# Kernel tuning notes

Measured on AMD Instinct MI355X. Metric: run time of the kernel, lower is better.

## Reference

```python
import jax, jax.numpy as jnp
import numpy as np

B, L, D = 2, 1024, 768
DEPTH, DI, N, K, R, FF = 6, 1536, 16, 4, 48, 3072  # d_inner=2*D, d_state, d_conv, dt_rank=D//16, ff=4*D


def setup_inputs() -> dict:
    key = jax.random.key(0)
    ks = iter(jax.random.split(key, 24))
    def rn(shape, sc=0.02):
        return jax.random.normal(next(ks), shape, dtype=jnp.float32) * sc
    return dict(
        x=rn((B, L, D), 1.0),
        ln1_w=jnp.ones((DEPTH, D), jnp.float32), ln1_b=jnp.zeros((DEPTH, D), jnp.float32),
        ln2_w=jnp.ones((DEPTH, D), jnp.float32), ln2_b=jnp.zeros((DEPTH, D), jnp.float32),
        in_w=rn((DEPTH, 2, 2 * DI, D)),
        conv_w=rn((DEPTH, 2, DI, K), 0.1), conv_b=jnp.zeros((DEPTH, 2, DI), jnp.float32),
        xproj_w=rn((DEPTH, 2, R + 2 * N, DI)),
        dtproj_w=rn((DEPTH, 2, DI, R), 0.1),
        dtproj_b=rn((DEPTH, 2, DI), 0.1),
        A_log=jnp.broadcast_to(jnp.log(jnp.arange(1, N + 1, dtype=jnp.float32)), (DEPTH, 2, DI, N)) + jnp.zeros((DEPTH, 2, DI, N), jnp.float32),
        D_param=jnp.ones((DEPTH, 2, DI), jnp.float32),
        out_w=rn((DEPTH, 2, D, DI)),
        mlp_w1=rn((DEPTH, FF, D)), mlp_b1=jnp.zeros((DEPTH, FF), jnp.float32),
        mlp_w2=rn((DEPTH, D, FF)), mlp_b2=jnp.zeros((DEPTH, D), jnp.float32),
    )


def _ln(x, w, b, eps=1e-5):
    m = x.mean(-1, keepdims=True)
    v = jnp.var(x, axis=-1, keepdims=True)
    return (x - m) * jax.lax.rsqrt(v + eps) * w + b


def _silu(x):
    return x * jax.nn.sigmoid(x)


def _mamba(x, in_w, conv_w, conv_b, xproj_w, dtproj_w, dtproj_b, A_log, Dp, out_w):
    b = x.shape[0]
    xz = jnp.einsum('bld,ed->ble', x, in_w)                    # (B,L,2*DI)
    xp, z = jnp.split(xz, 2, axis=-1)
    xt = jnp.transpose(xp, (0, 2, 1))                           # (B,DI,L)
    xc = jax.lax.conv_general_dilated(xt, conv_w[:, None, :], (1,), [(K - 1, 0)],
                                      dimension_numbers=('NCH', 'OIH', 'NCH'),
                                      feature_group_count=DI)   # causal depthwise conv
    xc = _silu(xc + conv_b[None, :, None])
    xc = jnp.transpose(xc, (0, 2, 1))                           # (B,L,DI)
    xdbl = jnp.einsum('bld,ed->ble', xc, xproj_w)               # (B,L,R+2N)
    dt_lr = xdbl[..., :R]                                       # low-rank dt (B,L,R)
    Bs = xdbl[..., R:R + N]
    Cs = xdbl[..., R + N:]
    dt = jax.nn.softplus(jnp.einsum('blr,dr->bld', dt_lr, dtproj_w) + dtproj_b)  # (B,L,DI)
    A = -jnp.exp(A_log)                                          # (DI,N)

    def step(h, inp):
        dt_t, b_t, c_t, x_t = inp                                # (B,DI),(B,N),(B,N),(B,DI)
        dA = jnp.exp(dt_t[:, :, None] * A)
        h = dA * h + dt_t[:, :, None] * b_t[:, None, :] * x_t[:, :, None]
        return h, jnp.einsum('bdn,bn->bd', h, c_t)

    h0 = jnp.zeros((b, DI, N), x.dtype)
    _, ys = jax.lax.scan(step, h0, (dt.transpose(1, 0, 2), Bs.transpose(1, 0, 2),
                                    Cs.transpose(1, 0, 2), xc.transpose(1, 0, 2)))
    y = ys.transpose(1, 0, 2) + xc * Dp                          # (B,L,DI)
    y = y * _silu(z)
    return jnp.einsum('bld,ed->ble', y, out_w), dt, dt_lr


def _encoder(x, ln1_w, ln1_b, ln2_w, ln2_b, in_w, conv_w, conv_b, xproj_w,
             dtproj_w, dtproj_b, A_log, D_param, out_w, mlp_w1, mlp_b1, mlp_w2, mlp_b2):
    residual = None
    xs, dts_all, dtlr_all = [], [], []
    for i in range(DEPTH):
        residual = x if residual is None else x + residual
        h = _ln(residual, ln1_w[i], ln1_b[i])
        def mp(d):
            return (in_w[i, d], conv_w[i, d], conv_b[i, d], xproj_w[i, d],
                    dtproj_w[i, d], dtproj_b[i, d], A_log[i, d], D_param[i, d], out_w[i, d])
        xf, dt_f, dtlr_f = _mamba(h, *mp(0))
        xr, dt_b, dtlr_b = _mamba(jnp.flip(h, 1), *mp(1))
        m = (xf + jnp.flip(xr, 1)) * 0.5                          # BiMamba average
        dts_all.append(jnp.stack([dt_f, dt_b], 0))                # dt_backward left reversed, as in source
        dtlr_all.append(jnp.stack([dtlr_f, dtlr_b], 0))
        residual = m + residual
        h2 = _ln(residual, ln2_w[i], ln2_b[i])
        hid = jax.nn.gelu(jnp.einsum('bld,fd->blf', h2, mlp_w1[i]) + mlp_b1[i], approximate=False)
        x = jnp.einsum('blf,df->bld', hid, mlp_w2[i]) + mlp_b2[i]
        xs.append(x)
    return x, jnp.stack(xs, 0), jnp.stack(dts_all, 0), jnp.stack(dtlr_all, 0)


def reference(x, ln1_w, ln1_b, ln2_w, ln2_b, in_w, conv_w, conv_b, xproj_w,
              dtproj_w, dtproj_b, A_log, D_param, out_w, mlp_w1, mlp_b1, mlp_w2, mlp_b2):
    return _encoder(x, ln1_w, ln1_b, ln2_w, ln2_b, in_w, conv_w, conv_b, xproj_w,
                    dtproj_w, dtproj_b, A_log, D_param, out_w, mlp_w1, mlp_b1, mlp_w2, mlp_b2)
```

## Files before the change

kernel.cpp:

```cpp
#include <hip/hip_runtime.h>
#include <cmath>

#define B_ 2
#define L_ 1024
#define D_ 768
#define DEPTH_ 6
#define DI_ 1536
#define NS_ 16
#define KC_ 4
#define R_ 48
#define FF_ 3072
#define BL_ (B_*L_)
#define XD_ 128
#define CH2_ 32
#define S_ 32

#define OUT_XS   ((size_t)BL_*D_)
#define OUT_DTS  (OUT_XS + (size_t)DEPTH_*BL_*D_)
#define OUT_DTLR (OUT_DTS + (size_t)DEPTH_*2*BL_*DI_)

typedef unsigned short u16;
typedef unsigned int u32;
typedef __bf16 bf16x8 __attribute__((ext_vector_type(8)));
typedef float f32x4 __attribute__((ext_vector_type(4)));

__device__ __forceinline__ float siluf(float x){ return x / (1.f + __expf(-x)); }
__device__ __forceinline__ float softplusf(float x){ return fmaxf(x,0.f) + log1pf(__expf(-fabsf(x))); }
__device__ __forceinline__ float geluf(float x){ return 0.5f*x*(1.f+erff(x*0.7071067811865475f)); }
__device__ __forceinline__ u32 f2bf(float f){
    u32 u = __float_as_uint(f);
    return (u + 0x7FFFu + ((u>>16)&1u)) >> 16;
}
__device__ __forceinline__ float bf2f(u16 v){ return __uint_as_float(((u32)v)<<16); }

__device__ __forceinline__ void cvt4(const float* __restrict__ in, u16* __restrict__ out, int i)
{
    float4 v = ((const float4*)in)[i];
    uint2 o;
    o.x = f2bf(v.x) | (f2bf(v.y) << 16);
    o.y = f2bf(v.z) | (f2bf(v.w) << 16);
    ((uint2*)out)[i] = o;
}

__global__ __launch_bounds__(256) void cvt_weights(
    const float* __restrict__ in_w, const float* __restrict__ out_w,
    const float* __restrict__ m1, const float* __restrict__ m2,
    const float* __restrict__ xp, const float* __restrict__ wdt,
    u16* __restrict__ w_in, u16* __restrict__ w_out, u16* __restrict__ w_m1,
    u16* __restrict__ w_m2, u16* __restrict__ w_xp, u16* __restrict__ w_dt)
{
    int seg = blockIdx.y;
    int i = blockIdx.x*256 + threadIdx.x;
    if (seg == 0) { if (i < 2*(2*DI_)*D_/4) cvt4(in_w, w_in, i); }
    else if (seg == 1) { if (i < 2*D_*DI_/4) cvt4(out_w, w_out, i); }
    else if (seg == 2) { if (i < FF_*D_/4) cvt4(m1, w_m1, i); }
    else if (seg == 3) { if (i < D_*FF_/4) cvt4(m2, w_m2, i); }
    else if (seg == 4) {
        if (i < 2*XD_*DI_/4) {
            int base = i*4;
            int k = base % DI_;
            int rr = (base/DI_) % XD_;
            int z = base/(DI_*XD_);
            uint2 o = {0u,0u};
            if (rr < 80) {
                float4 v = *(const float4*)&xp[((size_t)z*80 + rr)*DI_ + k];
                o.x = f2bf(v.x) | (f2bf(v.y) << 16);
                o.y = f2bf(v.z) | (f2bf(v.w) << 16);
            }
            ((uint2*)w_xp)[i] = o;
        }
    } else {
        if (i < 2*DI_*64/4) {
            int base = i*4;
            int c = base % 64;
            int r = (base/64) % DI_;
            int z = base/(64*DI_);
            uint2 o = {0u,0u};
            if (c < 48) {
                float4 v = *(const float4*)&wdt[((size_t)z*DI_ + r)*48 + c];
                o.x = f2bf(v.x) | (f2bf(v.y) << 16);
                o.y = f2bf(v.z) | (f2bf(v.w) << 16);
            }
            ((uint2*)w_dt)[i] = o;
        }
    }
}

template<int EPI, int OUTBF>
__global__ __launch_bounds__(256) void gemm_bf16(
    const u16* __restrict__ A, const u16* __restrict__ Bw,
    float* __restrict__ C, u16* __restrict__ Cbf, const float* __restrict__ bias,
    float* __restrict__ out2, int layer,
    int M, int N, int K, int KS, long aS, long bS, long cS, long biasS)
{
    const int zAll = blockIdx.z;
    const int sk = zAll % KS, zb = zAll / KS;
    A  += (size_t)zb * aS;
    Bw += (size_t)zb * bS;
    __shared__ u16 As[128*64];
    __shared__ u16 Bs[128*64];
    const int tid = threadIdx.x;
    const int w = tid >> 6, l = tid & 63;
    const int wr = w >> 1, wc = w & 1;
    const int row0 = blockIdx.x * 128, col0 = blockIdx.y * 128;
    const int Ksl = K / KS;
    const int kbeg = sk * Ksl;
    const int srow = l >> 3;
    const int scol = (l & 7) * 8;
    f32x4 acc[4][4] = {};
    for (int k0 = kbeg; k0 < kbeg + Ksl; k0 += 64) {
        #pragma unroll
        for (int c = 0; c < 4; ++c) {
            int chunk = w*4 + c;
            const u16* ga = A + (size_t)(row0 + chunk*8 + srow) * K + (k0 + scol);
            __builtin_amdgcn_global_load_lds(
                (const __attribute__((address_space(1))) void*)ga,
                (__attribute__((address_space(3))) void*)(As + chunk*512), 16, 0, 0);
            const u16* gb = Bw + (size_t)(col0 + chunk*8 + srow) * K + (k0 + scol);
            __builtin_amdgcn_global_load_lds(
                (const __attribute__((address_space(1))) void*)gb,
                (__attribute__((address_space(3))) void*)(Bs + chunk*512), 16, 0, 0);
        }
        __syncthreads();
        #pragma unroll
        for (int kk = 0; kk < 64; kk += 32) {
            bf16x8 af[4], bfr[4];
            #pragma unroll
            for (int m = 0; m < 4; ++m)
                af[m] = *(const bf16x8*)(As + (wr*64 + m*16 + (l&15))*64 + kk + (l>>4)*8);
            #pragma unroll
            for (int n = 0; n < 4; ++n)
                bfr[n] = *(const bf16x8*)(Bs + (wc*64 + n*16 + (l&15))*64 + kk + (l>>4)*8);
            #pragma unroll
            for (int m = 0; m < 4; ++m)
                #pragma unroll
                for (int n = 0; n < 4; ++n)
                    acc[m][n] = __builtin_amdgcn_mfma_f32_16x16x32_bf16(af[m], bfr[n], acc[m][n], 0, 0, 0);
        }
        __syncthreads();
    }
    if (KS > 1) {
        float* Cp = C + (size_t)(zb*KS + sk) * cS;
        #pragma unroll
        for (int m = 0; m < 4; ++m)
            #pragma unroll
            for (int j = 0; j < 4; ++j) {
                int r = row0 + wr*64 + m*16 + (l>>4)*4 + j;
                #pragma unroll
                for (int n = 0; n < 4; ++n) {
                    int col = col0 + wc*64 + n*16 + (l&15);
                    Cp[(size_t)r*N + col] = acc[m][n][j];
                }
            }
    } else {
        #pragma unroll
        for (int m = 0; m < 4; ++m)
            #pragma unroll
            for (int j = 0; j < 4; ++j) {
                int r = row0 + wr*64 + m*16 + (l>>4)*4 + j;
                #pragma unroll
                for (int n = 0; n < 4; ++n) {
                    int col = col0 + wc*64 + n*16 + (l&15);
                    float v = acc[m][n][j];
                    if (EPI == 2) {
                        Cbf[(size_t)zb*cS + (size_t)r*N + col] = (u16)f2bf(geluf(v + bias[col]));
                    } else if (EPI == 4) {
                        v = softplusf(v + bias[(size_t)zb*biasS + col]);
                        int b = r / L_, p = r % L_;
                        int t = zb ? (L_-1-p) : p;
                        out2[((((size_t)layer*2+zb)*B_ + b)*L_ + t)*DI_ + col] = v;
                    } else if (OUTBF) {
                        Cbf[(size_t)zb*cS + (size_t)r*N + col] = (u16)f2bf(v);
                    } else {
                        C[(size_t)zb*cS + (size_t)r*N + col] = v;
                    }
                }
            }
    }
}

__global__ __launch_bounds__(256) void xpred_dtlr(
    const float* __restrict__ part, float* __restrict__ xdbl,
    u16* __restrict__ dtlr_bf, float* __restrict__ out, int layer)
{
    int idx = blockIdx.x*256 + threadIdx.x;
    if (idx >= 2*BL_*XD_) return;
    int c = idx % XD_;
    int bl = (idx/XD_) % BL_;
    int z = idx/(XD_*BL_);
    const float* p8 = part + ((size_t)z*8)*BL_*XD_ + (size_t)bl*XD_ + c;
    float s = 0.f;
    #pragma unroll
    for (int sk = 0; sk < 8; ++sk) s += p8[(size_t)sk*BL_*XD_];
    xdbl[idx] = s;
    if (c < 64) dtlr_bf[((size_t)z*BL_ + bl)*64 + c] = (u16)f2bf(c < 48 ? s : 0.f);
    if (c < 48) {
        int b = bl / L_, p = bl % L_;
        int t = z ? (L_-1-p) : p;
        out[OUT_DTLR + ((((size_t)layer*2+z)*B_ + b)*L_ + t)*R_ + c] = s;
    }
}

__global__ __launch_bounds__(256) void ln_res_kernel(
    const float* __restrict__ xprev, float* __restrict__ residual,
    u16* __restrict__ hout, const float* __restrict__ w,
    const float* __restrict__ bia)
{
    int row = blockIdx.x; int tid = threadIdx.x;
    __shared__ float sbuf[8];
    float v[3]; float s=0.f, ss=0.f;
    size_t base = (size_t)row*D_;
    #pragma unroll
    for (int j=0;j<3;j++){
        int c = tid + j*256;
        float x = xprev[base+c];
        v[j]=x; s+=x; ss+=x*x;
        residual[base+c] = x;
    }
    for (int off=32; off; off>>=1){ s += __shfl_down(s,off); ss += __shfl_down(ss,off); }
    int wid = tid>>6, lane = tid&63;
    if (lane==0){ sbuf[wid]=s; sbuf[4+wid]=ss; }
    __syncthreads();
    if (tid==0){
        float S=sbuf[0]+sbuf[1]+sbuf[2]+sbuf[3];
        float SS=sbuf[4]+sbuf[5]+sbuf[6]+sbuf[7];
        float mean = S/(float)D_;
        float var = SS/(float)D_ - mean*mean;
        sbuf[0]=mean; sbuf[1]=rsqrtf(var+1e-5f);
    }
    __syncthreads();
    float mean=sbuf[0], inv=sbuf[1];
    #pragma unroll
    for (int j=0;j<3;j++){
        int c = tid + j*256;
        hout[base+c] = (u16)f2bf((v[j]-mean)*inv*w[c]+bia[c]);
    }
}

__global__ __launch_bounds__(256) void merge_ln_kernel(
    const float* __restrict__ part, float* __restrict__ residual,
    u16* __restrict__ h2, const float* __restrict__ w, const float* __restrict__ bia)
{
    int row = blockIdx.x; int tid = threadIdx.x;
    const size_t MN = (size_t)BL_*D_;
    __shared__ float sbuf[8];
    float v[3]; float s=0.f, ss=0.f;
    size_t base = (size_t)row*D_;
    #pragma unroll
    for (int j=0;j<3;j++){
        int c = tid + j*256;
        float o = part[base+c] + part[MN+base+c] + part[2*MN+base+c] + part[3*MN+base+c];
        float x = residual[base+c] + 0.5f*o;
        v[j]=x; s+=x; ss+=x*x;
        residual[base+c] = x;
    }
    for (int off=32; off; off>>=1){ s += __shfl_down(s,off); ss += __shfl_down(ss,off); }
    int wid = tid>>6, lane = tid&63;
    if (lane==0){ sbuf[wid]=s; sbuf[4+wid]=ss; }
    __syncthreads();
    if (tid==0){
        float S=sbuf[0]+sbuf[1]+sbuf[2]+sbuf[3];
        float SS=sbuf[4]+sbuf[5]+sbuf[6]+sbuf[7];
        float mean = S/(float)D_;
        float var = SS/(float)D_ - mean*mean;
        sbuf[0]=mean; sbuf[1]=rsqrtf(var+1e-5f);
    }
    __syncthreads();
    float mean=sbuf[0], inv=sbuf[1];
    #pragma unroll
    for (int j=0;j<3;j++){
        int c = tid + j*256;
        h2[base+c] = (u16)f2bf((v[j]-mean)*inv*w[c]+bia[c]);
    }
}

__global__ __launch_bounds__(256) void mlp2red_ln(
    const float* __restrict__ part, const float* __restrict__ b2,
    float* __restrict__ xs_out, float* __restrict__ residual,
    u16* __restrict__ hout, const float* __restrict__ w, const float* __restrict__ bia)
{
    int row = blockIdx.x; int tid = threadIdx.x;
    const size_t MN = (size_t)BL_*D_;
    __shared__ float sbuf[8];
    float v[3]; float s=0.f, ss=0.f;
    size_t base = (size_t)row*D_;
    #pragma unroll
    for (int j=0;j<3;j++){
        int c = tid + j*256;
        float x = part[base+c] + part[MN+base+c] + part[2*MN+base+c] + part[3*MN+base+c] + b2[c];
        xs_out[base+c] = x;
        float r = residual[base+c] + x;
        residual[base+c] = r;
        v[j]=r; s+=r; ss+=r*r;
    }
    for (int off=32; off; off>>=1){ s += __shfl_down(s,off); ss += __shfl_down(ss,off); }
    int wid = tid>>6, lane = tid&63;
    if (lane==0){ sbuf[wid]=s; sbuf[4+wid]=ss; }
    __syncthreads();
    if (tid==0){
        float S=sbuf[0]+sbuf[1]+sbuf[2]+sbuf[3];
        float SS=sbuf[4]+sbuf[5]+sbuf[6]+sbuf[7];
        float mean = S/(float)D_;
        float var = SS/(float)D_ - mean*mean;
        sbuf[0]=mean; sbuf[1]=rsqrtf(var+1e-5f);
    }
    __syncthreads();
    float mean=sbuf[0], inv=sbuf[1];
    #pragma unroll
    for (int j=0;j<3;j++){
        int c = tid + j*256;
        hout[base+c] = (u16)f2bf((v[j]-mean)*inv*w[c]+bia[c]);
    }
}

__global__ __launch_bounds__(256) void mlp2red_final(
    const float* __restrict__ part, const float* __restrict__ b2,
    float* __restrict__ xs_out, float* __restrict__ out0)
{
    int idx = blockIdx.x*256 + threadIdx.x;
    if (idx >= BL_*D_) return;
    const size_t MN = (size_t)BL_*D_;
    int c = idx % D_;
    float x = part[idx] + part[MN+idx] + part[2*MN+idx] + part[3*MN+idx] + b2[c];
    xs_out[idx] = x;
    out0[idx] = x;
}

__global__ __launch_bounds__(256) void conv_silu_v(
    const u16* __restrict__ xz, const float* __restrict__ conv_w,
    const float* __restrict__ conv_b, u16* __restrict__ xc, int layer)
{
    const int NG = DI_/8;
    int idx = blockIdx.x*256 + threadIdx.x;
    if (idx >= 2*BL_*NG) return;
    int g = idx % NG;
    int bl = (idx / NG) % BL_;
    int dir = idx / (NG*BL_);
    int b = bl / L_, p = bl % L_;
    int d0 = g*8;
    const float* wp = conv_w + ((size_t)(layer*2+dir)*DI_ + d0)*KC_;
    float w[8][4];
    #pragma unroll
    for (int d = 0; d < 8; ++d) {
        float4 t = ((const float4*)wp)[d];
        w[d][0]=t.x; w[d][1]=t.y; w[d][2]=t.z; w[d][3]=t.w;
    }
    float acc[8];
    const float* bp = conv_b + (size_t)(layer*2+dir)*DI_ + d0;
    #pragma unroll
    for (int d = 0; d < 8; ++d) acc[d] = bp[d];
    const u16* xp = xz + (size_t)dir*BL_*2*DI_ + d0;
    #pragma unroll
    for (int k = 0; k < KC_; ++k) {
        int q = (dir == 0) ? (p - 3 + k) : (p + 3 - k);
        if (q < 0 || q >= L_) continue;
        uint4 raw = *(const uint4*)(xp + (size_t)(b*L_+q)*2*DI_);
        const u16* xv = (const u16*)&raw;
        #pragma unroll
        for (int d = 0; d < 8; ++d) acc[d] = fmaf(bf2f(xv[d]), w[d][k], acc[d]);
    }
    u16 o[8];
    #pragma unroll
    for (int d = 0; d < 8; ++d) o[d] = (u16)f2bf(siluf(acc[d]));
    *(uint4*)(xc + (size_t)dir*BL_*DI_ + (size_t)bl*DI_ + d0) = *(uint4*)o;
}

__global__ __launch_bounds__(256) void scan_part2(
    const float* __restrict__ dts, const u16* __restrict__ xc,
    const float* __restrict__ xdbl, const float* __restrict__ A_log,
    float* __restrict__ hp, float* __restrict__ Pp, int layer)
{
    int bid = blockIdx.x;
    int dblk = bid % (DI_/256);
    int chunk = (bid/(DI_/256)) % CH2_;
    int b = (bid/((DI_/256)*CH2_)) % B_;
    int dir = bid / ((DI_/256)*CH2_*B_);
    int tid = threadIdx.x;
    int d = dblk*256 + tid;
    __shared__ float sB[S_][16];
    for (int i = tid; i < S_*16; i += 256) {
        int s = i >> 4, n = i & 15;
        int sidx = chunk*S_ + s;
        int p = dir ? (L_-1-sidx) : sidx;
        sB[s][n] = xdbl[(size_t)dir*BL_*XD_ + (size_t)(b*L_+p)*XD_ + 48 + n];
    }
    __syncthreads();
    float Av[16];
    const float* Ap = A_log + (((size_t)layer*2+dir)*DI_ + d)*NS_;
    #pragma unroll
    for (int n = 0; n < 16; ++n) Av[n] = -__expf(Ap[n]);
    float h[16] = {};
    float P[16];
    #pragma unroll
    for (int n = 0; n < 16; ++n) P[n] = 1.f;
    const float* dtp = dts + ((((size_t)layer*2+dir)*B_ + b)*L_)*DI_ + d;
    const u16*  xcp = xc + (size_t)dir*BL_*DI_ + (size_t)b*L_*DI_ + d;
    #pragma unroll 2
    for (int s = 0; s < S_; ++s) {
        int sidx = chunk*S_ + s;
        int p = dir ? (L_-1-sidx) : sidx;
        float dtv = dtp[(size_t)sidx*DI_];
        float xv  = bf2f(xcp[(size_t)p*DI_]);
        float u = dtv * xv;
        #pragma unroll
        for (int n = 0; n < 16; ++n) {
            float dA = __expf(dtv*Av[n]);
            P[n] *= dA;
            h[n] = fmaf(dA, h[n], u*sB[s][n]);
        }
    }
    size_t o = (((size_t)(dir*B_+b)*CH2_ + chunk)*DI_ + d)*16;
    #pragma unroll
    for (int n = 0; n < 16; n += 4) {
        *(float4*)&hp[o+n] = make_float4(h[n],h[n+1],h[n+2],h[n+3]);
        *(float4*)&Pp[o+n] = make_float4(P[n],P[n+1],P[n+2],P[n+3]);
    }
}

__global__ __launch_bounds__(256) void scan_combine(
    float* __restrict__ hp, const float* __restrict__ Pp)
{
    int bid = blockIdx.x;
    int seg = bid % (DI_*16/256);
    int b = (bid/(DI_*16/256)) % B_;
    int dir = bid / ((DI_*16/256)*B_);
    int idx = seg*256 + threadIdx.x;
    size_t base = ((size_t)(dir*B_+b)*CH2_)*DI_*16 + idx;
    float h = 0.f;
    for (int c = 0; c < CH2_; ++c) {
        size_t i = base + (size_t)c*DI_*16;
        float Pv = Pp[i], hl = hp[i];
        hp[i] = h;
        h = fmaf(Pv, h, hl);
    }
}

__global__ __launch_bounds__(256) void scan_final2(
    const float* __restrict__ dts, const u16* __restrict__ xc,
    const float* __restrict__ xdbl, const float* __restrict__ A_log,
    const float* __restrict__ hp, const u16* __restrict__ xz,
    const float* __restrict__ Dp, u16* __restrict__ yb, int layer)
{
    int bid = blockIdx.x;
    int dblk = bid % (DI_/256);
    int chunk = (bid/(DI_/256)) % CH2_;
    int b = (bid/((DI_/256)*CH2_)) % B_;
    int dir = bid / ((DI_/256)*CH2_*B_);
    int tid = threadIdx.x;
    int d = dblk*256 + tid;
    __shared__ float sB[S_][16], sC[S_][16];
    for (int i = tid; i < S_*16*2; i += 256) {
        int which = i >= S_*16;
        int j = i & (S_*16-1);
        int s = j >> 4, n = j & 15;
        int sidx = chunk*S_ + s;
        int p = dir ? (L_-1-sidx) : sidx;
        float v = xdbl[(size_t)dir*BL_*XD_ + (size_t)(b*L_+p)*XD_ + (which?64:48) + n];
        if (which) sC[s][n] = v; else sB[s][n] = v;
    }
    __syncthreads();
    float Av[16];
    const float* Ap = A_log + (((size_t)layer*2+dir)*DI_ + d)*NS_;
    #pragma unroll
    for (int n = 0; n < 16; ++n) Av[n] = -__expf(Ap[n]);
    float h[16];
    {
        size_t o = (((size_t)(dir*B_+b)*CH2_ + chunk)*DI_ + d)*16;
        #pragma unroll
        for (int n = 0; n < 16; n += 4) {
            float4 t = *(const float4*)&hp[o+n];
            h[n]=t.x; h[n+1]=t.y; h[n+2]=t.z; h[n+3]=t.w;
        }
    }
    float Dpv = Dp[(size_t)(layer*2+dir)*DI_ + d];
    const float* dtp = dts + ((((size_t)layer*2+dir)*B_ + b)*L_)*DI_ + d;
    const u16*  xcp = xc + (size_t)dir*BL_*DI_ + (size_t)b*L_*DI_ + d;
    const u16*  zp  = xz + (size_t)dir*BL_*2*DI_ + (size_t)b*L_*2*DI_ + DI_ + d;
    u16* yp = yb + (size_t)dir*BL_*DI_ + (size_t)b*L_*DI_ + d;
    #pragma unroll 2
    for (int s = 0; s < S_; ++s) {
        int sidx = chunk*S_ + s;
        int p = dir ? (L_-1-sidx) : sidx;
        float dtv = dtp[(size_t)sidx*DI_];
        float xv  = bf2f(xcp[(size_t)p*DI_]);
        float u = dtv * xv;
        float y = 0.f;
        #pragma unroll
        for (int n = 0; n < 16; ++n) {
            float dA = __expf(dtv*Av[n]);
            h[n] = fmaf(dA, h[n], u*sB[s][n]);
            y = fmaf(h[n], sC[s][n], y);
        }
        float z = bf2f(zp[(size_t)p*2*DI_]);
        float v = y + xv*Dpv;
        yp[(size_t)p*DI_] = (u16)f2bf(v * siluf(z));
    }
}

extern "C" void kernel_launch(void* const* d_in, const int* in_sizes, int n_in,
                              void* d_out, int out_size, void* d_ws, size_t ws_size,
                              hipStream_t stream)
{
    const float* x_in    = (const float*)d_in[0];
    const float* ln1_w   = (const float*)d_in[1];
    const float* ln1_b   = (const float*)d_in[2];
    const float* ln2_w   = (const float*)d_in[3];
    const float* ln2_b   = (const float*)d_in[4];
    const float* in_w    = (const float*)d_in[5];
    const float* conv_w  = (const float*)d_in[6];
    const float* conv_b  = (const float*)d_in[7];
    const float* xproj_w = (const float*)d_in[8];
    const float* dtproj_w= (const float*)d_in[9];
    const float* dtproj_b= (const float*)d_in[10];
    const float* A_log   = (const float*)d_in[11];
    const float* D_param = (const float*)d_in[12];
    const float* out_w   = (const float*)d_in[13];
    const float* mlp_w1  = (const float*)d_in[14];
    const float* mlp_b1  = (const float*)d_in[15];
    const float* mlp_w2  = (const float*)d_in[16];
    const float* mlp_b2  = (const float*)d_in[17];

    float* out = (float*)d_out;
    char* base = (char*)d_ws;
    float* res    = (float*)base;  base += (size_t)BL_*D_*4;
    u16*   xz     = (u16*)base;    base += (size_t)2*BL_*2*DI_*2;
    u16*   xc_bf  = (u16*)base;    base += (size_t)2*BL_*DI_*2;
    float* xdbl   = (float*)base;  base += (size_t)2*BL_*XD_*4;
    u16*   dtlr_bf= (u16*)base;    base += (size_t)2*BL_*64*2;
    float* hp     = (float*)base;  base += (size_t)2*B_*CH2_*DI_*16*4;
    float* part   = (float*)base;  base += (size_t)4*BL_*D_*4;
    u16*   yb_bf  = (u16*)base;    base += (size_t)2*BL_*DI_*2;
    u16*   h_bf   = (u16*)base;    base += (size_t)BL_*D_*2;
    u16*   h2_bf  = (u16*)base;    base += (size_t)BL_*D_*2;
    u16*   hid_bf = (u16*)base;    base += (size_t)BL_*FF_*2;
    u16*   w_in   = (u16*)base;    base += (size_t)2*(2*DI_)*D_*2;
    u16*   w_out  = (u16*)base;    base += (size_t)2*D_*DI_*2;
    u16*   w_m1   = (u16*)base;    base += (size_t)FF_*D_*2;
    u16*   w_m2   = (u16*)base;    base += (size_t)D_*FF_*2;
    u16*   w_xp   = (u16*)base;    base += (size_t)2*XD_*DI_*2;
    u16*   w_dt   = (u16*)base;    base += (size_t)2*DI_*64*2;

    float* Pp = part;
    float* dts_base = out + OUT_DTS;

    ln_res_kernel<<<BL_, 256, 0, stream>>>(x_in, res, h_bf, ln1_w, ln1_b);

    for (int i = 0; i < DEPTH_; ++i) {
        cvt_weights<<<dim3(4608, 6), 256, 0, stream>>>(
            in_w  + (size_t)i*2*(2*DI_)*D_, out_w + (size_t)i*2*D_*DI_,
            mlp_w1+ (size_t)i*FF_*D_,       mlp_w2+ (size_t)i*D_*FF_,
            xproj_w + (size_t)i*2*80*DI_,   dtproj_w + (size_t)i*2*DI_*48,
            w_in, w_out, w_m1, w_m2, w_xp, w_dt);

        dim3 gIn(BL_/128, (2*DI_)/128, 2);
        gemm_bf16<0,1><<<gIn, 256, 0, stream>>>(h_bf, w_in, nullptr, xz, nullptr, nullptr, 0,
            BL_, 2*DI_, D_, 1, 0L, (long)(2*DI_)*D_, (long)BL_*2*DI_, 0L);

        conv_silu_v<<<(2*BL_*(DI_/8)+255)/256, 256, 0, stream>>>(xz, conv_w, conv_b, xc_bf, i);

        dim3 gXp(BL_/128, 1, 2*8);
        gemm_bf16<0,0><<<gXp, 256, 0, stream>>>(xc_bf, w_xp, part, nullptr, nullptr, nullptr, 0,
            BL_, XD_, DI_, 8, (long)BL_*DI_, (long)XD_*DI_, (long)BL_*XD_, 0L);
        xpred_dtlr<<<(2*BL_*XD_+255)/256, 256, 0, stream>>>(part, xdbl, dtlr_bf, out, i);

        dim3 gDt(BL_/128, DI_/128, 2);
        gemm_bf16<4,0><<<gDt, 256, 0, stream>>>(dtlr_bf, w_dt, nullptr, nullptr,
            dtproj_b + (size_t)i*2*DI_, dts_base, i,
            BL_, DI_, 64, 1, (long)BL_*64, (long)DI_*64, 0L, (long)DI_);

        scan_part2<<<2*B_*CH2_*(DI_/256), 256, 0, stream>>>(dts_base, xc_bf, xdbl, A_log, hp, Pp, i);
        scan_combine<<<2*B_*(DI_*16/256), 256, 0, stream>>>(hp, Pp);
        scan_final2<<<2*B_*CH2_*(DI_/256), 256, 0, stream>>>(dts_base, xc_bf, xdbl, A_log, hp,
            xz, D_param, yb_bf, i);

        dim3 gOut(BL_/128, D_/128, 2*2);
        gemm_bf16<0,0><<<gOut, 256, 0, stream>>>(yb_bf, w_out, part, nullptr, nullptr, nullptr, 0,
            BL_, D_, DI_, 2, (long)BL_*DI_, (long)D_*DI_, (long)BL_*D_, 0L);
        merge_ln_kernel<<<BL_, 256, 0, stream>>>(part, res, h2_bf,
            ln2_w + (size_t)i*D_, ln2_b + (size_t)i*D_);

        dim3 gM1(BL_/128, FF_/128, 1);
        gemm_bf16<2,1><<<gM1, 256, 0, stream>>>(h2_bf, w_m1, nullptr, hid_bf,
            mlp_b1 + (size_t)i*FF_, nullptr, 0, BL_, FF_, D_, 1, 0L, 0L, (long)BL_*FF_, 0L);

        dim3 gM2(BL_/128, D_/128, 4);
        gemm_bf16<0,0><<<gM2, 256, 0, stream>>>(hid_bf, w_m2, part, nullptr, nullptr, nullptr, 0,
            BL_, D_, FF_, 4, 0L, 0L, (long)BL_*D_, 0L);

        if (i < DEPTH_-1) {
            mlp2red_ln<<<BL_, 256, 0, stream>>>(part, mlp_b2 + (size_t)i*D_,
                out + OUT_XS + (size_t)i*BL_*D_, res, h_bf,
                ln1_w + (size_t)(i+1)*D_, ln1_b + (size_t)(i+1)*D_);
        } else {
            mlp2red_final<<<(BL_*D_+255)/256, 256, 0, stream>>>(part, mlp_b2 + (size_t)i*D_,
                out + OUT_XS + (size_t)i*BL_*D_, out);
        }
    }
}
```

Before: 1.780 ms.

## Double-buffer GEMM LDS tiles with XOR swizzle and merge in-proj directions

```diff
diff --git a/kernel.cpp b/kernel.cpp
--- a/kernel.cpp
+++ b/kernel.cpp
@@ -14,6 +14,7 @@
 #define XD_ 128
 #define CH2_ 32
 #define S_ 32
+#define NXZ_ (2*2*DI_)
 
 #define OUT_XS   ((size_t)BL_*D_)
 #define OUT_DTS  (OUT_XS + (size_t)DEPTH_*BL_*D_)
@@ -86,6 +87,27 @@
     }
 }
 
+__device__ __forceinline__ void stage_tile(
+    const u16* __restrict__ G, u16* lds, int row0, int ldK, int k0, int w, int l)
+{
+    const int sub = l >> 3;
+    const int cg  = (l & 7) ^ sub;
+    #pragma unroll
+    for (int c = 0; c < 4; ++c) {
+        int chunk = w*4 + c;
+        const u16* g = G + (size_t)(row0 + chunk*8 + sub) * ldK + k0 + cg*8;
+        __builtin_amdgcn_global_load_lds(
+            (const __attribute__((address_space(1))) void*)g,
+            (__attribute__((address_space(3))) void*)(lds + chunk*512), 16, 0, 0);
+    }
+}
+
+__device__ __forceinline__ bf16x8 ldfrag(const u16* lds, int row, int kk2, int l)
+{
+    int chunk = (kk2*4 + (l>>4)) ^ (l & 7);
+    return *(const bf16x8*)(lds + row*64 + chunk*8);
+}
+
 template<int EPI, int OUTBF>
 __global__ __launch_bounds__(256) void gemm_bf16(
     const u16* __restrict__ A, const u16* __restrict__ Bw,
@@ -97,48 +119,50 @@
     const int sk = zAll % KS, zb = zAll / KS;
     A  += (size_t)zb * aS;
     Bw += (size_t)zb * bS;
-    __shared__ u16 As[128*64];
-    __shared__ u16 Bs[128*64];
+    __shared__ u16 As[2*128*64];
+    __shared__ u16 Bs[2*128*64];
     const int tid = threadIdx.x;
     const int w = tid >> 6, l = tid & 63;
     const int wr = w >> 1, wc = w & 1;
     const int row0 = blockIdx.x * 128, col0 = blockIdx.y * 128;
     const int Ksl = K / KS;
     const int kbeg = sk * Ksl;
-    const int srow = l >> 3;
-    const int scol = (l & 7) * 8;
+    const int nt = Ksl / 64;
     f32x4 acc[4][4] = {};
-    for (int k0 = kbeg; k0 < kbeg + Ksl; k0 += 64) {
-        #pragma unroll
-        for (int c = 0; c < 4; ++c) {
-            int chunk = w*4 + c;
-            const u16* ga = A + (size_t)(row0 + chunk*8 + srow) * K + (k0 + scol);
-            __builtin_amdgcn_global_load_lds(
-                (const __attribute__((address_space(1))) void*)ga,
-                (__attribute__((address_space(3))) void*)(As + chunk*512), 16, 0, 0);
-            const u16* gb = Bw + (size_t)(col0 + chunk*8 + srow) * K + (k0 + scol);
-            __builtin_amdgcn_global_load_lds(
-                (const __attribute__((address_space(1))) void*)gb,
-                (__attribute__((address_space(3))) void*)(Bs + chunk*512), 16, 0, 0);
+
+    stage_tile(A, As, row0, K, kbeg, w, l);
+    stage_tile(Bw, Bs, col0, K, kbeg, w, l);
+    __syncthreads();
+
+    for (int t = 0; t < nt; ++t) {
+        const int cur = t & 1;
+        if (t + 1 < nt) {
+            stage_tile(A, As + (cur^1)*8192, row0, K, kbeg + (t+1)*64, w, l);
+            stage_tile(Bw, Bs + (cur^1)*8192, col0, K, kbeg + (t+1)*64, w, l);
+        }
+        const u16* Ab = As + cur*8192;
+        const u16* Bb = Bs + cur*8192;
+        bf16x8 bfr[4][2];
+        #pragma unroll
+        for (int n = 0; n < 4; ++n)
+            #pragma unroll
+            for (int kk2 = 0; kk2 < 2; ++kk2)
+                bfr[n][kk2] = ldfrag(Bb, wc*64 + n*16 + (l&15), kk2, l);
+        #pragma unroll
+        for (int m = 0; m < 4; ++m) {
+            bf16x8 a0 = ldfrag(Ab, wr*64 + m*16 + (l&15), 0, l);
+            bf16x8 a1 = ldfrag(Ab, wr*64 + m*16 + (l&15), 1, l);
+            __builtin_amdgcn_s_setprio(1);
+            #pragma unroll
+            for (int n = 0; n < 4; ++n) {
+                acc[m][n] = __builtin_amdgcn_mfma_f32_16x16x32_bf16(a0, bfr[n][0], acc[m][n], 0, 0, 0);
+                acc[m][n] = __builtin_amdgcn_mfma_f32_16x16x32_bf16(a1, bfr[n][1], acc[m][n], 0, 0, 0);
+            }
+            __builtin_amdgcn_s_setprio(0);
         }
         __syncthreads();
-        #pragma unroll
-        for (int kk = 0; kk < 64; kk += 32) {
-            bf16x8 af[4], bfr[4];
-            #pragma unroll
-            for (int m = 0; m < 4; ++m)
-                af[m] = *(const bf16x8*)(As + (wr*64 + m*16 + (l&15))*64 + kk + (l>>4)*8);
-            #pragma unroll
-            for (int n = 0; n < 4; ++n)
-                bfr[n] = *(const bf16x8*)(Bs + (wc*64 + n*16 + (l&15))*64 + kk + (l>>4)*8);
-            #pragma unroll
-            for (int m = 0; m < 4; ++m)
-                #pragma unroll
-                for (int n = 0; n < 4; ++n)
-                    acc[m][n] = __builtin_amdgcn_mfma_f32_16x16x32_bf16(af[m], bfr[n], acc[m][n], 0, 0, 0);
-        }
-        __syncthreads();
-    }
+    }
+
     if (KS > 1) {
         float* Cp = C + (size_t)(zb*KS + sk) * cS;
         #pragma unroll
@@ -167,8 +191,8 @@
                     } else if (EPI == 4) {
                         v = softplusf(v + bias[(size_t)zb*biasS + col]);
                         int b = r / L_, p = r % L_;
-                        int t = zb ? (L_-1-p) : p;
-                        out2[((((size_t)layer*2+zb)*B_ + b)*L_ + t)*DI_ + col] = v;
+                        int tt = zb ? (L_-1-p) : p;
+                        out2[((((size_t)layer*2+zb)*B_ + b)*L_ + tt)*DI_ + col] = v;
                     } else if (OUTBF) {
                         Cbf[(size_t)zb*cS + (size_t)r*N + col] = (u16)f2bf(v);
                     } else {
@@ -349,12 +373,12 @@
     const float* bp = conv_b + (size_t)(layer*2+dir)*DI_ + d0;
     #pragma unroll
     for (int d = 0; d < 8; ++d) acc[d] = bp[d];
-    const u16* xp = xz + (size_t)dir*BL_*2*DI_ + d0;
+    const u16* xp = xz + dir*(2*DI_) + d0;
     #pragma unroll
     for (int k = 0; k < KC_; ++k) {
         int q = (dir == 0) ? (p - 3 + k) : (p + 3 - k);
         if (q < 0 || q >= L_) continue;
-        uint4 raw = *(const uint4*)(xp + (size_t)(b*L_+q)*2*DI_);
+        uint4 raw = *(const uint4*)(xp + (size_t)(b*L_+q)*NXZ_);
         const u16* xv = (const u16*)&raw;
         #pragma unroll
         for (int d = 0; d < 8; ++d) acc[d] = fmaf(bf2f(xv[d]), w[d][k], acc[d]);
@@ -475,7 +499,7 @@
     float Dpv = Dp[(size_t)(layer*2+dir)*DI_ + d];
     const float* dtp = dts + ((((size_t)layer*2+dir)*B_ + b)*L_)*DI_ + d;
     const u16*  xcp = xc + (size_t)dir*BL_*DI_ + (size_t)b*L_*DI_ + d;
-    const u16*  zp  = xz + (size_t)dir*BL_*2*DI_ + (size_t)b*L_*2*DI_ + DI_ + d;
+    const u16*  zp  = xz + (size_t)b*L_*NXZ_ + dir*(2*DI_) + DI_ + d;
     u16* yp = yb + (size_t)dir*BL_*DI_ + (size_t)b*L_*DI_ + d;
     #pragma unroll 2
     for (int s = 0; s < S_; ++s) {
@@ -491,7 +515,7 @@
             h[n] = fmaf(dA, h[n], u*sB[s][n]);
             y = fmaf(h[n], sC[s][n], y);
         }
-        float z = bf2f(zp[(size_t)p*2*DI_]);
+        float z = bf2f(zp[(size_t)p*NXZ_]);
         float v = y + xv*Dpv;
         yp[(size_t)p*DI_] = (u16)f2bf(v * siluf(z));
     }
@@ -523,7 +547,7 @@
     float* out = (float*)d_out;
     char* base = (char*)d_ws;
     float* res    = (float*)base;  base += (size_t)BL_*D_*4;
-    u16*   xz     = (u16*)base;    base += (size_t)2*BL_*2*DI_*2;
+    u16*   xz     = (u16*)base;    base += (size_t)BL_*NXZ_*2;
     u16*   xc_bf  = (u16*)base;    base += (size_t)2*BL_*DI_*2;
     float* xdbl   = (float*)base;  base += (size_t)2*BL_*XD_*4;
     u16*   dtlr_bf= (u16*)base;    base += (size_t)2*BL_*64*2;
@@ -552,9 +576,9 @@
             xproj_w + (size_t)i*2*80*DI_,   dtproj_w + (size_t)i*2*DI_*48,
             w_in, w_out, w_m1, w_m2, w_xp, w_dt);
 
-        dim3 gIn(BL_/128, (2*DI_)/128, 2);
+        dim3 gIn(BL_/128, NXZ_/128, 1);
         gemm_bf16<0,1><<<gIn, 256, 0, stream>>>(h_bf, w_in, nullptr, xz, nullptr, nullptr, 0,
-            BL_, 2*DI_, D_, 1, 0L, (long)(2*DI_)*D_, (long)BL_*2*DI_, 0L);
+            BL_, NXZ_, D_, 1, 0L, 0L, 0L, 0L);
 
         conv_silu_v<<<(2*BL_*(DI_/8)+255)/256, 256, 0, stream>>>(xz, conv_w, conv_b, xc_bf, i);
 
```

Measured after the change: 1.654 ms. 1.08x faster.
